# Kernel optimization log

Hardware: AMD Instinct MI355X
Metric: run time of the kernel (lower is better)

Reference implementation:

```python
import jax, jax.numpy as jnp
import numpy as np

N_HEAD = 8
HIDDENS = 512
NEG_INF = -1e9


def setup_inputs() -> dict:
    key = jax.random.key(0)
    ks = jax.random.split(key, 10)
    B, L, KVP, QP, H, W = 8, 1024, 512, 512, 32, 32
    s = 0.02  # init scale
    return {
        "v": jax.random.normal(ks[0], (B, L, KVP), jnp.float32),
        "k": jax.random.normal(ks[1], (B, L, KVP), jnp.float32),
        "q": jax.random.normal(ks[2], (B, QP, H, W), jnp.float32),
        "mask": jax.random.randint(ks[3], (B, 1, 1, L), 0, 2) > 0,
        "Wv": jax.random.normal(ks[4], (HIDDENS, KVP), jnp.float32) * s,
        "bv": jnp.zeros((HIDDENS,), jnp.float32),
        "Wk": jax.random.normal(ks[5], (HIDDENS, KVP), jnp.float32) * s,
        "bk": jnp.zeros((HIDDENS,), jnp.float32),
        "Wq": jax.random.normal(ks[6], (HIDDENS, QP), jnp.float32) * s,
        "bq": jnp.zeros((HIDDENS,), jnp.float32),
        "Wm": jax.random.normal(ks[7], (512, HIDDENS), jnp.float32) * s,
        "bm": jnp.zeros((512,), jnp.float32),
    }


def reference(v, k, q, mask, Wv, bv, Wk, bk, Wq, bq, Wm, bm):
    B, _, H, W = q.shape
    nh, dh = N_HEAD, HIDDENS // N_HEAD
    # k/v linear projections -> [B, nh, L, dh]
    vh = (v @ Wv.T + bv).reshape(B, -1, nh, dh).transpose(0, 2, 1, 3)
    kh = (k @ Wk.T + bk).reshape(B, -1, nh, dh).transpose(0, 2, 1, 3)
    # q 1x1 conv projection -> [B, hiddens, H, W] -> [B, nh, HW, dh]
    qp = jnp.einsum('bchw,oc->bohw', q, Wq) + bq[None, :, None, None]
    qh = qp.reshape(B, nh, dh, H * W).transpose(0, 1, 3, 2)
    # attention: scores fully materialized [B, nh, HW, L]
    scores = jnp.einsum('bnqd,bnkd->bnqk', qh, kh) / jnp.sqrt(jnp.float32(dh))
    scores = jnp.where(mask, NEG_INF, scores)
    att = jax.nn.softmax(scores, axis=-1)  # dropout omitted (eval mode)
    out = jnp.einsum('bnqk,bnkd->bnqd', att, vh)
    # [B, nh, HW, dh] -> [B, hiddens, H, W]
    out = out.transpose(0, 1, 3, 2).reshape(B, HIDDENS, H, W)
    out = jnp.einsum('bchw,oc->bohw', out, Wm) + bm[None, :, None, None]
    return jax.nn.relu(out)
```

## Files before the change

### kernel.cpp

```cpp
#include <hip/hip_runtime.h>

typedef __attribute__((ext_vector_type(8))) __bf16 bf16x8;
typedef __attribute__((ext_vector_type(4))) float  f32x4;

#define SCALE_Q 0.1803368801111204f
#define THR_L2  11.541560327111708f

__device__ __forceinline__ unsigned short f2bf(float f) {
    unsigned int u = __builtin_bit_cast(unsigned int, f);
    u += 0x7fffu + ((u >> 16) & 1u);
    return (unsigned short)(u >> 16);
}
__device__ __forceinline__ unsigned int pack2(float a, float b) {
    return (unsigned int)f2bf(a) | ((unsigned int)f2bf(b) << 16);
}

__device__ __forceinline__ int idxW(int row, int ch) {
    return row * 512 + (((ch & ~7) | ((ch ^ row) & 7)) << 3);
}
__device__ __forceinline__ int swz8(int row, int chunk) {
    return row * 64 + ((chunk ^ (row & 7)) << 3);
}
__device__ __forceinline__ bf16x8 fragld(const unsigned short* lds, int row, int kk, int lane) {
    return *(const bf16x8*)(lds + swz8(row, kk * 4 + (lane >> 4)));
}

__global__ __launch_bounds__(256) void ck_w(const float* __restrict__ Wv, const float* __restrict__ Wk,
                                            const float* __restrict__ Wq, const float* __restrict__ Wm,
                                            unsigned short* __restrict__ Wp) {
    int tid = threadIdx.x, lane = tid & 63;
    int gw = blockIdx.x * 4 + (tid >> 6);
    int w = gw >> 9, rem = gw & 511;
    int nb = rem >> 4, kb = rem & 15;
    const float* src = (w == 0) ? Wv : (w == 1) ? Wk : (w == 2) ? Wq : Wm;
    const float* gp = src + (size_t)(nb * 16 + (lane & 15)) * 512 + kb * 32 + (lane >> 4) * 8;
    float4 v0 = *(const float4*)gp, v1 = *(const float4*)(gp + 4);
    uint4 o;
    o.x = pack2(v0.x, v0.y); o.y = pack2(v0.z, v0.w);
    o.z = pack2(v1.x, v1.y); o.w = pack2(v1.z, v1.w);
    *(uint4*)(Wp + ((size_t)w << 18) + ((size_t)((nb * 16 + kb) * 64 + lane)) * 8) = o;
}

__global__ __launch_bounds__(256, 2) void g_proj(const float* __restrict__ kin,
                                                 const float* __restrict__ vin,
                                                 const float* __restrict__ qin,
                                                 const unsigned short* __restrict__ Wp,
                                                 const float* __restrict__ bk,
                                                 const float* __restrict__ bv,
                                                 const float* __restrict__ bq,
                                                 unsigned short* __restrict__ kh,
                                                 unsigned short* __restrict__ vh,
                                                 unsigned short* __restrict__ qh) {
    __shared__ alignas(16) unsigned short As[64 * 512];
    int tid = threadIdx.x, lane = tid & 63, wv = tid >> 6;
    int pid = blockIdx.x;
    int srcSel = (pid < 128) ? 0 : (pid < 256) ? 1 : 2;

    if (srcSel < 2) {
        int panel = (srcSel == 0) ? pid : pid - 128;
        const float* src = ((srcSel == 0) ? kin : vin) + (size_t)panel * 64 * 512;
#pragma unroll
        for (int it = 0; it < 16; ++it) {
            int id = it * 256 + tid, row = id >> 6, ch = id & 63;
            const float* gp = src + (size_t)row * 512 + ch * 8;
            float4 a0 = *(const float4*)gp, a1 = *(const float4*)(gp + 4);
            uint4 w;
            w.x = pack2(a0.x, a0.y); w.y = pack2(a0.z, a0.w);
            w.z = pack2(a1.x, a1.y); w.w = pack2(a1.z, a1.w);
            *(uint4*)(&As[idxW(row, ch)]) = w;
        }
    } else {
        int qi = pid - 256, b = qi >> 4, pp = qi & 15;
        const float* src = qin + (size_t)b * 512 * 1024 + pp * 64;
#pragma unroll
        for (int cc = 0; cc < 8; ++cc) {
            int c0 = cc * 64 + (tid >> 4) * 4;
            int pl = (tid & 15) * 4;
            float rr[4][4];
#pragma unroll
            for (int i = 0; i < 4; ++i) {
                float4 t4 = *(const float4*)(src + (size_t)(c0 + i) * 1024 + pl);
                rr[i][0] = t4.x; rr[i][1] = t4.y; rr[i][2] = t4.z; rr[i][3] = t4.w;
            }
#pragma unroll
            for (int j = 0; j < 4; ++j) {
                int row = pl + j, chunk = c0 >> 3, off = c0 & 7;
                uint2 w2;
                w2.x = pack2(rr[0][j], rr[1][j]);
                w2.y = pack2(rr[2][j], rr[3][j]);
                *(uint2*)(&As[row * 512 + (((chunk & ~7) | ((chunk ^ row) & 7)) << 3) + off]) = w2;
            }
        }
    }
    __syncthreads();

    int wsel = (srcSel == 0) ? 1 : (srcSel == 1) ? 0 : 2;
    const unsigned short* Wb = Wp + ((size_t)wsel << 18);
    f32x4 acc[4][8] = {};
#pragma unroll 2
    for (int kb = 0; kb < 16; ++kb) {
        bf16x8 af[4];
#pragma unroll
        for (int i = 0; i < 4; ++i)
            af[i] = *(const bf16x8*)(&As[idxW(i * 16 + (lane & 15), kb * 4 + (lane >> 4))]);
#pragma unroll
        for (int j = 0; j < 8; ++j) {
            bf16x8 bf8 = *(const bf16x8*)(Wb + ((size_t)(((wv * 8 + j) * 16 + kb) * 64 + lane)) * 8);
#pragma unroll
            for (int i = 0; i < 4; ++i)
                acc[i][j] = __builtin_amdgcn_mfma_f32_16x16x32_bf16(af[i], bf8, acc[i][j], 0, 0, 0);
        }
    }

    if (srcSel < 2) {
        int panel = (srcSel == 0) ? pid : pid - 128;
        unsigned short* dst = (srcSel == 0) ? kh : vh;
        const float* bias = (srcSel == 0) ? bk : bv;
#pragma unroll
        for (int j = 0; j < 8; ++j) {
            int o = wv * 128 + j * 16 + (lane & 15);
            float bb = bias[o];
            int n = o >> 6, d = o & 63;
#pragma unroll
            for (int i = 0; i < 4; ++i)
#pragma unroll
                for (int reg = 0; reg < 4; ++reg) {
                    int r = panel * 64 + i * 16 + ((lane >> 4) << 2) + reg;
                    dst[(((size_t)((r >> 10) * 8 + n)) * 1024 + (r & 1023)) * 64 + d] =
                        f2bf(acc[i][j][reg] + bb);
                }
        }
    } else {
        int qi = pid - 256, b = qi >> 4, pp = qi & 15;
#pragma unroll
        for (int j = 0; j < 8; ++j) {
            int o = wv * 128 + j * 16 + (lane & 15);
            float bb = bq[o];
            int n = o >> 6, d = o & 63;
#pragma unroll
            for (int i = 0; i < 4; ++i)
#pragma unroll
                for (int reg = 0; reg < 4; ++reg) {
                    int p = pp * 64 + i * 16 + ((lane >> 4) << 2) + reg;
                    qh[(((size_t)(b * 8 + n)) * 1024 + p) * 64 + d] =
                        f2bf((acc[i][j][reg] + bb) * SCALE_Q);
                }
        }
    }
}

__device__ __forceinline__ void stage_direct_bf16(unsigned short* lds, const unsigned short* g,
                                                  int ldg, int tid) {
#pragma unroll
    for (int s = 0; s < 2; ++s) {
        int idx = tid + s * 256;
        int row = idx >> 3, c = idx & 7;
        uint4 v = *(const uint4*)(g + (size_t)row * ldg + c * 8);
        *(uint4*)(lds + swz8(row, c)) = v;
    }
}
__device__ __forceinline__ void stage_trans_bf16(unsigned short* lds, const unsigned short* g,
                                                 int ldg, int tid) {
    int tk = (tid >> 4) * 4;
    int tn = (tid & 15) * 4;
    unsigned short rr[4][4];
#pragma unroll
    for (int i = 0; i < 4; ++i) {
        ushort4 v = *(const ushort4*)(g + (size_t)(tk + i) * ldg + tn);
        rr[i][0] = v.x; rr[i][1] = v.y; rr[i][2] = v.z; rr[i][3] = v.w;
    }
#pragma unroll
    for (int j = 0; j < 4; ++j) {
        int row = tn + j;
        ushort4 w4;
        w4.x = rr[0][j]; w4.y = rr[1][j]; w4.z = rr[2][j]; w4.w = rr[3][j];
        int off = row * 64 + (((tk >> 3) ^ (row & 7)) << 3) + (tk & 7);
        *(ushort4*)(lds + off) = w4;
    }
}

__global__ __launch_bounds__(256) void k_attn(unsigned short* qa,
                                              const unsigned short* __restrict__ kh,
                                              const unsigned short* __restrict__ vh,
                                              const int* __restrict__ mask) {
    __shared__ alignas(16) unsigned short Qs[64 * 64];
    __shared__ alignas(16) unsigned short Ks[64 * 64];
    __shared__ alignas(16) unsigned short Vs[64 * 64];
    __shared__ alignas(16) unsigned short Ps[4][16 * 64];
    int tid = threadIdx.x, lane = tid & 63, wv = tid >> 6;
    int bn = blockIdx.x;
    int b = bn >> 3;
    int p0 = blockIdx.y * 64;
    const unsigned short* kbase = kh + ((size_t)bn) * 1024 * 64;
    const unsigned short* vbase = vh + ((size_t)bn) * 1024 * 64;
    const int* mbase = mask + (size_t)b * 1024;

    stage_direct_bf16(Qs, qa + (((size_t)bn) * 1024 + p0) * 64, 64, tid);
    __syncthreads();
    bf16x8 aq0 = fragld(Qs, wv * 16 + (lane & 15), 0, lane);
    bf16x8 aq1 = fragld(Qs, wv * 16 + (lane & 15), 1, lane);

    float mrow[4], lrow[4];
    f32x4 o4[4] = {};
#pragma unroll
    for (int r = 0; r < 4; ++r) { mrow[r] = -3e38f; lrow[r] = 0.f; }

    for (int t = 0; t < 16; ++t) {
        int l0 = t * 64;
        __syncthreads();
        stage_direct_bf16(Ks, kbase + (size_t)l0 * 64, 64, tid);
        stage_trans_bf16(Vs, vbase + (size_t)l0 * 64, 64, tid);
        __syncthreads();

        f32x4 s[4] = {};
#pragma unroll
        for (int j = 0; j < 4; ++j) {
            bf16x8 bk0 = fragld(Ks, j * 16 + (lane & 15), 0, lane);
            bf16x8 bk1 = fragld(Ks, j * 16 + (lane & 15), 1, lane);
            s[j] = __builtin_amdgcn_mfma_f32_16x16x32_bf16(aq0, bk0, s[j], 0, 0, 0);
            s[j] = __builtin_amdgcn_mfma_f32_16x16x32_bf16(aq1, bk1, s[j], 0, 0, 0);
        }
#pragma unroll
        for (int j = 0; j < 4; ++j) {
            if (mbase[l0 + j * 16 + (lane & 15)] != 0) {
#pragma unroll
                for (int reg = 0; reg < 4; ++reg) s[j][reg] = -1e9f;
            }
        }
        float mx[4];
        bool ok = true;
#pragma unroll
        for (int reg = 0; reg < 4; ++reg) {
            float m_ = fmaxf(fmaxf(s[0][reg], s[1][reg]), fmaxf(s[2][reg], s[3][reg]));
#pragma unroll
            for (int off = 1; off < 16; off <<= 1) m_ = fmaxf(m_, __shfl_xor(m_, off, 64));
            mx[reg] = m_;
            ok = ok && (m_ <= mrow[reg] + THR_L2);
        }
        float pvv[4][4];
        if (__all(ok)) {
#pragma unroll
            for (int reg = 0; reg < 4; ++reg) {
                float sum = 0.f;
#pragma unroll
                for (int j = 0; j < 4; ++j) {
                    float p = exp2f(s[j][reg] - mrow[reg]);
                    pvv[j][reg] = p; sum += p;
                }
#pragma unroll
                for (int off = 1; off < 16; off <<= 1) sum += __shfl_xor(sum, off, 64);
                lrow[reg] += sum;
            }
        } else {
            float corr[4];
#pragma unroll
            for (int reg = 0; reg < 4; ++reg) {
                float mnew = fmaxf(mrow[reg], mx[reg]);
                corr[reg] = exp2f(mrow[reg] - mnew);
                float sum = 0.f;
#pragma unroll
                for (int j = 0; j < 4; ++j) {
                    float p = exp2f(s[j][reg] - mnew);
                    pvv[j][reg] = p; sum += p;
                }
#pragma unroll
                for (int off = 1; off < 16; off <<= 1) sum += __shfl_xor(sum, off, 64);
                lrow[reg] = lrow[reg] * corr[reg] + sum;
                mrow[reg] = mnew;
            }
#pragma unroll
            for (int jd = 0; jd < 4; ++jd)
#pragma unroll
                for (int reg = 0; reg < 4; ++reg) o4[jd][reg] *= corr[reg];
        }
        unsigned short* Pw = Ps[wv];
#pragma unroll
        for (int j = 0; j < 4; ++j) {
            int c = j * 16 + (lane & 15);
#pragma unroll
            for (int reg = 0; reg < 4; ++reg) {
                int pr = ((lane >> 4) << 2) + reg;
                Pw[pr * 64 + (((c >> 3) ^ (pr & 7)) << 3) + (c & 7)] = f2bf(pvv[j][reg]);
            }
        }
#pragma unroll
        for (int kk = 0; kk < 2; ++kk) {
            bf16x8 ap = fragld(Pw, (lane & 15), kk, lane);
#pragma unroll
            for (int jd = 0; jd < 4; ++jd) {
                bf16x8 bvf = fragld(Vs, jd * 16 + (lane & 15), kk, lane);
                o4[jd] = __builtin_amdgcn_mfma_f32_16x16x32_bf16(ap, bvf, o4[jd], 0, 0, 0);
            }
        }
    }
    float inv[4];
#pragma unroll
    for (int reg = 0; reg < 4; ++reg) inv[reg] = 1.f / lrow[reg];
    unsigned short* Ow = Ps[wv];
#pragma unroll
    for (int jd = 0; jd < 4; ++jd) {
        int d = jd * 16 + (lane & 15);
        int ch = d >> 3, doff = d & 7;
#pragma unroll
        for (int reg = 0; reg < 4; ++reg) {
            int pr = ((lane >> 4) << 2) + reg;
            Ow[pr * 64 + ((ch ^ (pr & 7)) << 3) + doff] = f2bf(o4[jd][reg] * inv[reg]);
        }
    }
    size_t base = ((size_t)bn * 16 + blockIdx.y) * 4096;
#pragma unroll
    for (int h = 0; h < 2; ++h) {
        int p = lane & 15;
        int ch = h * 4 + (lane >> 4);
        uint4 w = *(const uint4*)(&Ow[p * 64 + ((ch ^ (p & 7)) << 3)]);
        *(uint4*)(qa + base + (size_t)(wv * 2 + h) * 512 + (size_t)lane * 8) = w;
    }
}

__global__ __launch_bounds__(256, 2) void g_final(const unsigned short* __restrict__ aP,
                                                  const unsigned short* __restrict__ Wm8,
                                                  const float* __restrict__ bm,
                                                  float* __restrict__ out) {
    int tid = threadIdx.x, lane = tid & 63, wv = tid >> 6;
    int wr = wv >> 1, wc = wv & 1;
    int b = blockIdx.z, m0 = blockIdx.x * 128, n0 = blockIdx.y * 128;
    int onb = m0 / 16 + wr * 4;
    int pnb = n0 / 16 + wc * 4;
    f32x4 acc[4][4] = {};
#pragma unroll 2
    for (int kb = 0; kb < 16; ++kb) {
        int nh = kb >> 1, h = kb & 1, bn = b * 8 + nh;
        bf16x8 af[4], bf8[4];
#pragma unroll
        for (int i = 0; i < 4; ++i)
            af[i] = *(const bf16x8*)(Wm8 + ((size_t)(((onb + i) * 16 + kb) * 64 + lane)) * 8);
#pragma unroll
        for (int j = 0; j < 4; ++j) {
            int pb = pnb + j;
            bf8[j] = *(const bf16x8*)(aP + ((size_t)bn * 16 + (pb >> 2)) * 4096 +
                                      (size_t)((pb & 3) * 2 + h) * 512 + (size_t)lane * 8);
        }
#pragma unroll
        for (int i = 0; i < 4; ++i)
#pragma unroll
            for (int j = 0; j < 4; ++j)
                acc[i][j] = __builtin_amdgcn_mfma_f32_16x16x32_bf16(af[i], bf8[j], acc[i][j], 0, 0, 0);
    }
#pragma unroll
    for (int i = 0; i < 4; ++i)
#pragma unroll
        for (int reg = 0; reg < 4; ++reg) {
            int o = m0 + wr * 64 + i * 16 + ((lane >> 4) << 2) + reg;
            float bb = bm[o];
#pragma unroll
            for (int j = 0; j < 4; ++j) {
                int p = n0 + wc * 64 + j * 16 + (lane & 15);
                out[((size_t)(b * 512 + o)) * 1024 + p] = fmaxf(acc[i][j][reg] + bb, 0.f);
            }
        }
}

extern "C" void kernel_launch(void* const* d_in, const int* in_sizes, int n_in,
                              void* d_out, int out_size, void* d_ws, size_t ws_size,
                              hipStream_t stream) {
    const float* v  = (const float*)d_in[0];
    const float* k  = (const float*)d_in[1];
    const float* q  = (const float*)d_in[2];
    const int*   mask = (const int*)d_in[3];
    const float* Wv = (const float*)d_in[4];
    const float* bv = (const float*)d_in[5];
    const float* Wk = (const float*)d_in[6];
    const float* bk = (const float*)d_in[7];
    const float* Wq = (const float*)d_in[8];
    const float* bq = (const float*)d_in[9];
    const float* Wm = (const float*)d_in[10];
    const float* bm = (const float*)d_in[11];
    float* out = (float*)d_out;

    const size_t E = (size_t)8 * 8 * 1024 * 64;
    unsigned short* kh = (unsigned short*)d_ws;
    unsigned short* vh = kh + E;
    unsigned short* qh = vh + E;
    unsigned short* Wp = qh + E;

    dim3 blk(256);
    ck_w  <<<512, blk, 0, stream>>>(Wv, Wk, Wq, Wm, Wp);
    g_proj<<<384, blk, 0, stream>>>(k, v, q, Wp, bk, bv, bq, kh, vh, qh);
    k_attn<<<dim3(64, 16), blk, 0, stream>>>(qh, kh, vh, mask);
    g_final<<<dim3(4, 8, 8), blk, 0, stream>>>(qh, Wp + 3 * 262144, bm, out);
}
```

Measured before the change: 238.4 us.

## Register-prefetch next K/V tiles and mask, reuse Q LDS for P

The attention kernel now loads the next K/V tile and the mask values into registers while the current tile is being computed, then writes them to LDS at the start of the next iteration. This hides global load latency behind the MFMA and softmax work. The P buffer now reuses each wave's own slice of the Q LDS region, which cuts LDS use and may raise occupancy. The lazy-rescale branch of the online softmax is dropped in favour of always applying the correction. The projection GEMM also hoists all eight weight-fragment loads ahead of the MFMAs, which costs more registers.

```diff
diff --git a/kernel.cpp b/kernel.cpp
--- a/kernel.cpp
+++ b/kernel.cpp
@@ -4,7 +4,6 @@
 typedef __attribute__((ext_vector_type(4))) float  f32x4;
 
 #define SCALE_Q 0.1803368801111204f
-#define THR_L2  11.541560327111708f
 
 __device__ __forceinline__ unsigned short f2bf(float f) {
     unsigned int u = __builtin_bit_cast(unsigned int, f);
@@ -99,17 +98,18 @@
     f32x4 acc[4][8] = {};
 #pragma unroll 2
     for (int kb = 0; kb < 16; ++kb) {
-        bf16x8 af[4];
+        bf16x8 af[4], bf8[8];
+#pragma unroll
+        for (int j = 0; j < 8; ++j)
+            bf8[j] = *(const bf16x8*)(Wb + ((size_t)(((wv * 8 + j) * 16 + kb) * 64 + lane)) * 8);
 #pragma unroll
         for (int i = 0; i < 4; ++i)
             af[i] = *(const bf16x8*)(&As[idxW(i * 16 + (lane & 15), kb * 4 + (lane >> 4))]);
 #pragma unroll
-        for (int j = 0; j < 8; ++j) {
-            bf16x8 bf8 = *(const bf16x8*)(Wb + ((size_t)(((wv * 8 + j) * 16 + kb) * 64 + lane)) * 8);
+        for (int j = 0; j < 8; ++j)
 #pragma unroll
             for (int i = 0; i < 4; ++i)
-                acc[i][j] = __builtin_amdgcn_mfma_f32_16x16x32_bf16(af[i], bf8, acc[i][j], 0, 0, 0);
-        }
+                acc[i][j] = __builtin_amdgcn_mfma_f32_16x16x32_bf16(af[i], bf8[j], acc[i][j], 0, 0, 0);
     }
 
     if (srcSel < 2) {
@@ -146,36 +146,6 @@
                         f2bf((acc[i][j][reg] + bb) * SCALE_Q);
                 }
         }
-    }
-}
-
-__device__ __forceinline__ void stage_direct_bf16(unsigned short* lds, const unsigned short* g,
-                                                  int ldg, int tid) {
-#pragma unroll
-    for (int s = 0; s < 2; ++s) {
-        int idx = tid + s * 256;
-        int row = idx >> 3, c = idx & 7;
-        uint4 v = *(const uint4*)(g + (size_t)row * ldg + c * 8);
-        *(uint4*)(lds + swz8(row, c)) = v;
-    }
-}
-__device__ __forceinline__ void stage_trans_bf16(unsigned short* lds, const unsigned short* g,
-                                                 int ldg, int tid) {
-    int tk = (tid >> 4) * 4;
-    int tn = (tid & 15) * 4;
-    unsigned short rr[4][4];
-#pragma unroll
-    for (int i = 0; i < 4; ++i) {
-        ushort4 v = *(const ushort4*)(g + (size_t)(tk + i) * ldg + tn);
-        rr[i][0] = v.x; rr[i][1] = v.y; rr[i][2] = v.z; rr[i][3] = v.w;
-    }
-#pragma unroll
-    for (int j = 0; j < 4; ++j) {
-        int row = tn + j;
-        ushort4 w4;
-        w4.x = rr[0][j]; w4.y = rr[1][j]; w4.z = rr[2][j]; w4.w = rr[3][j];
-        int off = row * 64 + (((tk >> 3) ^ (row & 7)) << 3) + (tk & 7);
-        *(ushort4*)(lds + off) = w4;
     }
 }
 
@@ -186,7 +156,6 @@
     __shared__ alignas(16) unsigned short Qs[64 * 64];
     __shared__ alignas(16) unsigned short Ks[64 * 64];
     __shared__ alignas(16) unsigned short Vs[64 * 64];
-    __shared__ alignas(16) unsigned short Ps[4][16 * 64];
     int tid = threadIdx.x, lane = tid & 63, wv = tid >> 6;
     int bn = blockIdx.x;
     int b = bn >> 3;
@@ -195,10 +164,32 @@
     const unsigned short* vbase = vh + ((size_t)bn) * 1024 * 64;
     const int* mbase = mask + (size_t)b * 1024;
 
-    stage_direct_bf16(Qs, qa + (((size_t)bn) * 1024 + p0) * 64, 64, tid);
+    {
+        const unsigned short* g = qa + (((size_t)bn) * 1024 + p0) * 64;
+#pragma unroll
+        for (int s = 0; s < 2; ++s) {
+            int idx = tid + s * 256, row = idx >> 3, c = idx & 7;
+            *(uint4*)(&Qs[swz8(row, c)]) = *(const uint4*)(g + (size_t)row * 64 + c * 8);
+        }
+    }
     __syncthreads();
     bf16x8 aq0 = fragld(Qs, wv * 16 + (lane & 15), 0, lane);
     bf16x8 aq1 = fragld(Qs, wv * 16 + (lane & 15), 1, lane);
+    unsigned short* Pw = &Qs[wv * 16 * 64];
+
+    int krow = tid >> 3, kch = tid & 7;
+    int vtk = (tid >> 4) * 4, vtn = (tid & 15) * 4;
+    uint4 kreg[2];
+    ushort4 vreg[4];
+    int mcur[4];
+#pragma unroll
+    for (int s = 0; s < 2; ++s)
+        kreg[s] = *(const uint4*)(kbase + (size_t)(krow + s * 32) * 64 + kch * 8);
+#pragma unroll
+    for (int i = 0; i < 4; ++i)
+        vreg[i] = *(const ushort4*)(vbase + (size_t)(vtk + i) * 64 + vtn);
+#pragma unroll
+    for (int j = 0; j < 4; ++j) mcur[j] = mbase[j * 16 + (lane & 15)];
 
     float mrow[4], lrow[4];
     f32x4 o4[4] = {};
@@ -206,11 +197,27 @@
     for (int r = 0; r < 4; ++r) { mrow[r] = -3e38f; lrow[r] = 0.f; }
 
     for (int t = 0; t < 16; ++t) {
-        int l0 = t * 64;
         __syncthreads();
-        stage_direct_bf16(Ks, kbase + (size_t)l0 * 64, 64, tid);
-        stage_trans_bf16(Vs, vbase + (size_t)l0 * 64, 64, tid);
+#pragma unroll
+        for (int s = 0; s < 2; ++s)
+            *(uint4*)(&Ks[swz8(krow + s * 32, kch)]) = kreg[s];
+#pragma unroll
+        for (int j = 0; j < 4; ++j) {
+            int row = vtn + j;
+            ushort4 w4;
+            w4.x = vreg[0][j]; w4.y = vreg[1][j]; w4.z = vreg[2][j]; w4.w = vreg[3][j];
+            *(ushort4*)(&Vs[row * 64 + (((vtk >> 3) ^ (row & 7)) << 3) + (vtk & 7)]) = w4;
+        }
         __syncthreads();
+        if (t < 15) {
+            int l1 = (t + 1) * 64;
+#pragma unroll
+            for (int s = 0; s < 2; ++s)
+                kreg[s] = *(const uint4*)(kbase + (size_t)(l1 + krow + s * 32) * 64 + kch * 8);
+#pragma unroll
+            for (int i = 0; i < 4; ++i)
+                vreg[i] = *(const ushort4*)(vbase + (size_t)(l1 + vtk + i) * 64 + vtn);
+        }
 
         f32x4 s[4] = {};
 #pragma unroll
@@ -222,58 +229,36 @@
         }
 #pragma unroll
         for (int j = 0; j < 4; ++j) {
-            if (mbase[l0 + j * 16 + (lane & 15)] != 0) {
+            if (mcur[j] != 0) {
 #pragma unroll
                 for (int reg = 0; reg < 4; ++reg) s[j][reg] = -1e9f;
             }
         }
-        float mx[4];
-        bool ok = true;
+        if (t < 15) {
+            int l1 = (t + 1) * 64;
+#pragma unroll
+            for (int j = 0; j < 4; ++j) mcur[j] = mbase[l1 + j * 16 + (lane & 15)];
+        }
+
+        float pvv[4][4], corr[4];
 #pragma unroll
         for (int reg = 0; reg < 4; ++reg) {
-            float m_ = fmaxf(fmaxf(s[0][reg], s[1][reg]), fmaxf(s[2][reg], s[3][reg]));
-#pragma unroll
-            for (int off = 1; off < 16; off <<= 1) m_ = fmaxf(m_, __shfl_xor(m_, off, 64));
-            mx[reg] = m_;
-            ok = ok && (m_ <= mrow[reg] + THR_L2);
-        }
-        float pvv[4][4];
-        if (__all(ok)) {
-#pragma unroll
-            for (int reg = 0; reg < 4; ++reg) {
-                float sum = 0.f;
-#pragma unroll
-                for (int j = 0; j < 4; ++j) {
-                    float p = exp2f(s[j][reg] - mrow[reg]);
-                    pvv[j][reg] = p; sum += p;
-                }
-#pragma unroll
-                for (int off = 1; off < 16; off <<= 1) sum += __shfl_xor(sum, off, 64);
-                lrow[reg] += sum;
-            }
-        } else {
-            float corr[4];
-#pragma unroll
-            for (int reg = 0; reg < 4; ++reg) {
-                float mnew = fmaxf(mrow[reg], mx[reg]);
-                corr[reg] = exp2f(mrow[reg] - mnew);
-                float sum = 0.f;
-#pragma unroll
-                for (int j = 0; j < 4; ++j) {
-                    float p = exp2f(s[j][reg] - mnew);
-                    pvv[j][reg] = p; sum += p;
-                }
-#pragma unroll
-                for (int off = 1; off < 16; off <<= 1) sum += __shfl_xor(sum, off, 64);
-                lrow[reg] = lrow[reg] * corr[reg] + sum;
-                mrow[reg] = mnew;
-            }
-#pragma unroll
-            for (int jd = 0; jd < 4; ++jd)
-#pragma unroll
-                for (int reg = 0; reg < 4; ++reg) o4[jd][reg] *= corr[reg];
-        }
-        unsigned short* Pw = Ps[wv];
+            float mx = fmaxf(fmaxf(s[0][reg], s[1][reg]), fmaxf(s[2][reg], s[3][reg]));
+#pragma unroll
+            for (int off = 1; off < 16; off <<= 1) mx = fmaxf(mx, __shfl_xor(mx, off, 64));
+            float mnew = fmaxf(mrow[reg], mx);
+            corr[reg] = exp2f(mrow[reg] - mnew);
+            mrow[reg] = mnew;
+            float sum = 0.f;
+#pragma unroll
+            for (int j = 0; j < 4; ++j) {
+                float p = exp2f(s[j][reg] - mnew);
+                pvv[j][reg] = p; sum += p;
+            }
+#pragma unroll
+            for (int off = 1; off < 16; off <<= 1) sum += __shfl_xor(sum, off, 64);
+            lrow[reg] = lrow[reg] * corr[reg] + sum;
+        }
 #pragma unroll
         for (int j = 0; j < 4; ++j) {
             int c = j * 16 + (lane & 15);
@@ -284,6 +269,10 @@
             }
         }
 #pragma unroll
+        for (int jd = 0; jd < 4; ++jd)
+#pragma unroll
+            for (int reg = 0; reg < 4; ++reg) o4[jd][reg] *= corr[reg];
+#pragma unroll
         for (int kk = 0; kk < 2; ++kk) {
             bf16x8 ap = fragld(Pw, (lane & 15), kk, lane);
 #pragma unroll
@@ -296,7 +285,7 @@
     float inv[4];
 #pragma unroll
     for (int reg = 0; reg < 4; ++reg) inv[reg] = 1.f / lrow[reg];
-    unsigned short* Ow = Ps[wv];
+    unsigned short* Ow = Pw;
 #pragma unroll
     for (int jd = 0; jd < 4; ++jd) {
         int d = jd * 16 + (lane & 15);
```

Result: faster. 224.4 us (-5.9%).
